# Kernel optimization log

Measured on AMD Instinct MI355X. Metric: run time of the kernel, lower is better.

## Reference

```python
import jax, jax.numpy as jnp
import numpy as np

N, D, N_CLASSES = 8192, 512, 128
POS_MARGIN = 1.0  # default path: sample_method=None, Dynamic_margin=None


def setup_inputs() -> dict:
    key = jax.random.key(0)
    k1, k2 = jax.random.split(key)
    x = jax.random.normal(k1, (N, D), dtype=jnp.float32)
    # metric-learning embeddings are L2-normalized so sim in [-1, 1]
    x = x / jnp.linalg.norm(x, axis=1, keepdims=True)
    targets = jax.random.randint(k2, (N,), 0, N_CLASSES, dtype=jnp.int64)
    return {"inputs": x, "targets": targets, "nonorm": 0}


def reference(inputs, targets, nonorm):
    n = inputs.shape[0]
    sim = jnp.matmul(inputs, inputs.T)                      # [n, n]
    same = targets[:, None] == targets[None, :]             # [n, n]
    pos_mask = same & (sim < POS_MARGIN)                    # drops self-sim == 1
    neg_mask = ~same

    # per-row masked log-sum-exp (sort in original is irrelevant to the sums)
    pos_sum = jnp.sum(jnp.where(pos_mask, jnp.exp(1.0 - sim), 0.0), axis=1)
    neg_sum = jnp.sum(jnp.where(neg_mask, jnp.exp(sim), 0.0), axis=1)
    pos_loss = jnp.log(pos_sum)
    neg_loss = jnp.log(neg_sum)

    has_neg = jnp.any(neg_mask, axis=1)                     # rows w/o negs are skipped
    loss = jnp.sum(jnp.where(has_neg, pos_loss + neg_loss, 0.0)) / n
    prec = jnp.mean(1.0 - has_neg.astype(jnp.float32))      # fraction of skipped rows

    # torch code reports means of the LAST row's pos/neg pairs
    last_pos = pos_mask[-1]
    last_neg = neg_mask[-1]
    mean_pos_sim = jnp.sum(jnp.where(last_pos, sim[-1], 0.0)) / jnp.sum(last_pos)
    mean_neg_sim = jnp.sum(jnp.where(last_neg, sim[-1], 0.0)) / jnp.sum(last_neg)
    return loss, prec, mean_pos_sim, mean_neg_sim
```

## Files before the change

kernel.cpp:

```cpp
#include <hip/hip_runtime.h>
#include <math.h>

#define N_ 8192
#define D_ 512
#define NC_ 128
#define T32 32
#define BK_ 64
#define KSTEPS 8

typedef __attribute__((ext_vector_type(8))) short bf16x8;
typedef __attribute__((ext_vector_type(4))) float f32x4;
typedef __attribute__((ext_vector_type(4))) unsigned short us4;

static __device__ __forceinline__ unsigned short f2bf(float f) {
    union { float f; unsigned u; } c; c.f = f;
    unsigned u = c.u;
    u += 0x7fffu + ((u >> 16) & 1u);
    return (unsigned short)(u >> 16);
}

__global__ __launch_bounds__(256) void k_pre(const float* __restrict__ x,
                                             unsigned short* __restrict__ xb,
                                             const int* __restrict__ tg,
                                             double* __restrict__ sim_last,
                                             int* __restrict__ hist32) {
    const int bid = blockIdx.x;
    const int tid = threadIdx.x;
    if (bid < 4096) {
        int i = bid * 256 + tid;
        float4 v = reinterpret_cast<const float4*>(x)[i];
        us4 o = { f2bf(v.x), f2bf(v.y), f2bf(v.z), f2bf(v.w) };
        reinterpret_cast<us4*>(xb)[i] = o;
    } else if (bid < 6144) {
        int j    = (bid - 4096) * 4 + (tid >> 6);
        int lane = tid & 63;
        const float* xl = x + (size_t)(N_ - 1) * D_;
        const float* xj = x + (size_t)j * D_;
        double acc = 0.0;
#pragma unroll
        for (int it = 0; it < 8; ++it) {
            int k = it * 64 + lane;
            acc += (double)xl[k] * (double)xj[k];
        }
#pragma unroll
        for (int m = 32; m >= 1; m >>= 1) acc += __shfl_xor(acc, m, 64);
        if (lane == 0) sim_last[j] = acc;
    } else {
        __shared__ int lh[NC_];
        int b = bid - 6144;
        if (tid < NC_) lh[tid] = 0;
        __syncthreads();
        atomicAdd(&lh[tg[b * 256 + tid]], 1);
        __syncthreads();
        if (tid < NC_) hist32[b * NC_ + tid] = lh[tid];
    }
}

__global__ __launch_bounds__(512, 2) void k_main(const unsigned short* __restrict__ xb,
                                                 const int* __restrict__ tg,
                                                 float* __restrict__ bufP,
                                                 float* __restrict__ bufN) {
    __shared__ alignas(16) unsigned short As0_[2 * 256 * 64];
    __shared__ alignas(16) unsigned short Bs0_[2 * 256 * 64];

    const int tid  = threadIdx.x;
    const int w    = tid >> 6;
    const int lane = tid & 63;
    const int q    = lane >> 4;
    const int l15  = lane & 15;
    const int wrow = w >> 2;
    const int wcol = w & 3;

    const int bswz = (blockIdx.x & 7) * 66 + (blockIdx.x >> 3);

    int rem = bswz;
    int it = 0;
    while (rem >= (T32 - it)) { rem -= (T32 - it); it++; }
    const int jt = it + rem;
    const int row0 = it * 256;
    const int col0 = jt * 256;

    auto stage_tile = [&](int p, int kt) {
        const int k0 = kt * BK_;
#pragma unroll
        for (int set = 0; set < 4; ++set) {
            int ls = set * 4096 + tid * 8;
            int r  = ls >> 6;
            int sl = (ls >> 3) & 7;
            int g  = sl ^ (r & 7);
            const unsigned short* ga = xb + (size_t)(row0 + r) * D_ + k0 + g * 8;
            const unsigned short* gb = xb + (size_t)(col0 + r) * D_ + k0 + g * 8;
            __builtin_amdgcn_global_load_lds(
                (const __attribute__((address_space(1))) void*)ga,
                (__attribute__((address_space(3))) void*)(As0_ + p * 16384 + set * 4096 + w * 512),
                16, 0, 0);
            __builtin_amdgcn_global_load_lds(
                (const __attribute__((address_space(1))) void*)gb,
                (__attribute__((address_space(3))) void*)(Bs0_ + p * 16384 + set * 4096 + w * 512),
                16, 0, 0);
        }
    };

    f32x4 acc[8][4];
#pragma unroll
    for (int mi = 0; mi < 8; ++mi)
#pragma unroll
        for (int ni = 0; ni < 4; ++ni)
            acc[mi][ni] = (f32x4){0.f, 0.f, 0.f, 0.f};

    auto compute_kc = [&](int p, int kc) {
        bf16x8 aF[8], bF[4];
#pragma unroll
        for (int mi = 0; mi < 8; ++mi) {
            int rA = wrow * 128 + mi * 16 + l15;
            int sl = (kc * 4 + q) ^ (rA & 7);
            aF[mi] = *reinterpret_cast<const bf16x8*>(As0_ + p * 16384 + rA * 64 + sl * 8);
        }
#pragma unroll
        for (int ni = 0; ni < 4; ++ni) {
            int rB = wcol * 64 + ni * 16 + l15;
            int sl = (kc * 4 + q) ^ (rB & 7);
            bF[ni] = *reinterpret_cast<const bf16x8*>(Bs0_ + p * 16384 + rB * 64 + sl * 8);
        }
        asm volatile("s_waitcnt lgkmcnt(0)" ::: "memory");
        __builtin_amdgcn_sched_barrier(0);
        __builtin_amdgcn_s_setprio(1);
#pragma unroll
        for (int mi = 0; mi < 8; ++mi)
#pragma unroll
            for (int ni = 0; ni < 4; ++ni)
                acc[mi][ni] = __builtin_amdgcn_mfma_f32_16x16x32_bf16(
                    aF[mi], bF[ni], acc[mi][ni], 0, 0, 0);
        __builtin_amdgcn_s_setprio(0);
    };

#define TILE(P, KS, DOSTAGE, VMN)                                         \
    do {                                                                  \
        asm volatile("s_waitcnt vmcnt(" #VMN ")" ::: "memory");           \
        __builtin_amdgcn_s_barrier();                                     \
        __builtin_amdgcn_sched_barrier(0);                                \
        compute_kc(P, 0);                                                 \
        compute_kc(P, 1);                                                 \
        __builtin_amdgcn_s_barrier();                                     \
        if (DOSTAGE) stage_tile(P, (KS) + 2);                             \
    } while (0)

    stage_tile(0, 0);
    stage_tile(1, 1);

    TILE(0, 0, 1, 8);
    TILE(1, 1, 1, 8);
    TILE(0, 2, 1, 8);
    TILE(1, 3, 1, 8);
    TILE(0, 4, 1, 8);
    TILE(1, 5, 1, 8);
    TILE(0, 6, 0, 8);
    TILE(1, 7, 0, 0);
#undef TILE

    int tC[4];
#pragma unroll
    for (int ni = 0; ni < 4; ++ni)
        tC[ni] = tg[col0 + wcol * 64 + ni * 16 + l15];

    float cps[4], cns[4];
#pragma unroll
    for (int ni = 0; ni < 4; ++ni) { cps[ni] = 0.f; cns[ni] = 0.f; }

    float* scr = (float*)As0_;

#pragma unroll
    for (int mi = 0; mi < 8; ++mi) {
        int tRv[4];
#pragma unroll
        for (int r = 0; r < 4; ++r)
            tRv[r] = tg[row0 + wrow * 128 + mi * 16 + q * 4 + r];
        float ps_[4] = {0.f, 0.f, 0.f, 0.f};
        float ns_[4] = {0.f, 0.f, 0.f, 0.f};
#pragma unroll
        for (int ni = 0; ni < 4; ++ni)
#pragma unroll
            for (int r = 0; r < 4; ++r) {
                float s = acc[mi][ni][r];
                bool same = (tRv[r] == tC[ni]);
                float e = __expf(same ? 1.0f - s : s);
                float pe = (same && (s < 1.0f)) ? e : 0.0f;
                float ne = same ? 0.0f : e;
                ps_[r] += pe; ns_[r] += ne;
                cps[ni] += pe; cns[ni] += ne;
            }
#pragma unroll
        for (int r = 0; r < 4; ++r) {
            float p = ps_[r];
            float n = ns_[r];
#pragma unroll
            for (int m = 1; m < 16; m <<= 1) {
                p += __shfl_xor(p, m, 64);
                n += __shfl_xor(n, m, 64);
            }
            if (l15 == 0) {
                int rloc = wrow * 128 + mi * 16 + q * 4 + r;
                scr[wcol * 256 + rloc]        = p;
                scr[1024 + wcol * 256 + rloc] = n;
            }
        }
    }

#pragma unroll
    for (int ni = 0; ni < 4; ++ni) {
        float p = cps[ni];
        float n = cns[ni];
        p += __shfl_xor(p, 16, 64); p += __shfl_xor(p, 32, 64);
        n += __shfl_xor(n, 16, 64); n += __shfl_xor(n, 32, 64);
        if (q == 0) {
            int cloc = wcol * 64 + ni * 16 + l15;
            scr[2048 + wrow * 256 + cloc] = p;
            scr[2560 + wrow * 256 + cloc] = n;
        }
    }
    __syncthreads();

    if (tid < 256) {
        int r = tid;
        size_t off = ((size_t)it * T32 + jt) * 256 + r;
        bufP[off] = scr[r] + scr[256 + r] + scr[512 + r] + scr[768 + r];
        bufN[off] = scr[1024 + r] + scr[1280 + r] + scr[1536 + r] + scr[1792 + r];
    } else if (jt != it) {
        int c = tid - 256;
        size_t off = ((size_t)jt * T32 + it) * 256 + c;
        bufP[off] = scr[2048 + c] + scr[2304 + c];
        bufN[off] = scr[2560 + c] + scr[2816 + c];
    }
}

__global__ __launch_bounds__(512) void k_post(const float* __restrict__ bufP,
                                              const float* __restrict__ bufN,
                                              const int* __restrict__ tg,
                                              const int* __restrict__ hist32,
                                              const double* __restrict__ sim_last,
                                              double* __restrict__ dpart,
                                              int* __restrict__ ipart) {
    __shared__ float sv[512];
    __shared__ int lh[NC_];
    __shared__ double Rd[512], Pd[512], Nd[512];
    __shared__ int Ri[512], Pc[512], Nc[512];
    const int rt  = blockIdx.x;
    const int tid = threadIdx.x;
    const int half = tid >> 8;
    const int r    = tid & 255;
    const float* buf  = half ? bufN : bufP;
    const float* base = buf + (size_t)rt * T32 * 256 + r;
    float s = 0.f;
#pragma unroll
    for (int o = 0; o < T32; ++o) s += base[o * 256];
    sv[tid] = s;
    if (tid < NC_) {
        int a = 0;
#pragma unroll
        for (int b = 0; b < 32; ++b) a += hist32[b * NC_ + tid];
        lh[tid] = a;
    }
    __syncthreads();
    double rd = 0.0, pd = 0.0, nd = 0.0;
    int ri = 0, pc = 0, nc = 0;
    if (tid < 256) {
        int row = rt * 256 + tid;
        bool ok = lh[tg[row]] < N_;
        rd = ok ? (double)(logf(sv[tid]) + logf(sv[256 + tid])) : 0.0;
        ri = ok ? 0 : 1;
        double sl = sim_last[row];
        int tlast = tg[N_ - 1];
        if (tg[row] == tlast) { if (sl < 1.0) { pd = sl; pc = 1; } }
        else                  { nd = sl; nc = 1; }
    }
    Rd[tid] = rd; Pd[tid] = pd; Nd[tid] = nd;
    Ri[tid] = ri; Pc[tid] = pc; Nc[tid] = nc;
    __syncthreads();
    for (int st = 256; st >= 1; st >>= 1) {
        if (tid < st) {
            Rd[tid] += Rd[tid + st]; Pd[tid] += Pd[tid + st]; Nd[tid] += Nd[tid + st];
            Ri[tid] += Ri[tid + st]; Pc[tid] += Pc[tid + st]; Nc[tid] += Nc[tid + st];
        }
        __syncthreads();
    }
    if (tid == 0) {
        dpart[rt] = Rd[0]; dpart[32 + rt] = Pd[0]; dpart[64 + rt] = Nd[0];
        ipart[rt] = Ri[0]; ipart[32 + rt] = Pc[0]; ipart[64 + rt] = Nc[0];
    }
}

__global__ __launch_bounds__(64) void k_fin(const double* __restrict__ dpart,
                                            const int* __restrict__ ipart,
                                            float* __restrict__ out) {
    int tid = threadIdx.x;
    double rd = tid < 32 ? dpart[tid]      : 0.0;
    double pd = tid < 32 ? dpart[32 + tid] : 0.0;
    double nd = tid < 32 ? dpart[64 + tid] : 0.0;
    int    ri = tid < 32 ? ipart[tid]      : 0;
    int    pc = tid < 32 ? ipart[32 + tid] : 0;
    int    nc = tid < 32 ? ipart[64 + tid] : 0;
#pragma unroll
    for (int m = 32; m >= 1; m >>= 1) {
        rd += __shfl_xor(rd, m, 64); pd += __shfl_xor(pd, m, 64);
        nd += __shfl_xor(nd, m, 64);
        ri += __shfl_xor(ri, m, 64); pc += __shfl_xor(pc, m, 64);
        nc += __shfl_xor(nc, m, 64);
    }
    if (tid == 0) {
        out[0] = (float)(rd / (double)N_);
        out[1] = (float)ri / (float)N_;
        out[2] = (float)(pd / (double)pc);
        out[3] = (float)(nd / (double)nc);
    }
}

extern "C" void kernel_launch(void* const* d_in, const int* in_sizes, int n_in,
                              void* d_out, int out_size, void* d_ws, size_t ws_size,
                              hipStream_t stream) {
    const float* x  = (const float*)d_in[0];
    const int*   tg = (const int*)d_in[1];
    char* ws = (char*)d_ws;

    unsigned short* xb = (unsigned short*)ws;
    const size_t XB = (size_t)N_ * D_ * 2;
    float*  bufP     = (float*)(ws + XB);
    float*  bufN     = (float*)(ws + XB + (1u << 20));
    double* sim_last = (double*)(ws + XB + (2u << 20));
    int*    hist32   = (int*)(ws + XB + (2u << 20) + 65536);
    double* dpart    = (double*)(ws + XB + (2u << 20) + 65536 + 16384);
    int*    ipart    = (int*)(ws + XB + (2u << 20) + 65536 + 16384 + 1024);

    const int nblk_tri = T32 * (T32 + 1) / 2;

    hipLaunchKernelGGL(k_pre, dim3(4096 + 2048 + 32), dim3(256), 0, stream,
                       x, xb, tg, sim_last, hist32);
    hipLaunchKernelGGL(k_main, dim3(nblk_tri), dim3(512), 0, stream, xb, tg, bufP, bufN);
    hipLaunchKernelGGL(k_post, dim3(T32), dim3(512), 0, stream,
                       bufP, bufN, tg, hist32, sim_last, dpart, ipart);
    hipLaunchKernelGGL(k_fin, dim3(1), dim3(64), 0, stream, dpart, ipart, (float*)d_out);
}
```

Before: 157.4 us.

## Fuse final reduction into k_post via atomics and relax k_main launch bounds

```diff
diff --git a/kernel.cpp b/kernel.cpp
--- a/kernel.cpp
+++ b/kernel.cpp
@@ -23,9 +23,18 @@
                                              unsigned short* __restrict__ xb,
                                              const int* __restrict__ tg,
                                              double* __restrict__ sim_last,
-                                             int* __restrict__ hist32) {
+                                             int* __restrict__ hist32,
+                                             double* __restrict__ gd,
+                                             int* __restrict__ gi) {
     const int bid = blockIdx.x;
     const int tid = threadIdx.x;
+    if (bid == 0 && tid == 0) {
+        atomicExch((unsigned long long*)&gd[0], 0ull);
+        atomicExch((unsigned long long*)&gd[1], 0ull);
+        atomicExch((unsigned long long*)&gd[2], 0ull);
+        atomicExch(&gi[0], 0); atomicExch(&gi[1], 0);
+        atomicExch(&gi[2], 0); atomicExch(&gi[3], 0);
+    }
     if (bid < 4096) {
         int i = bid * 256 + tid;
         float4 v = reinterpret_cast<const float4*>(x)[i];
@@ -56,7 +65,7 @@
     }
 }
 
-__global__ __launch_bounds__(512, 2) void k_main(const unsigned short* __restrict__ xb,
+__global__ __launch_bounds__(512, 1) void k_main(const unsigned short* __restrict__ xb,
                                                  const int* __restrict__ tg,
                                                  float* __restrict__ bufP,
                                                  float* __restrict__ bufN) {
@@ -142,6 +151,7 @@
         compute_kc(P, 0);                                                 \
         compute_kc(P, 1);                                                 \
         __builtin_amdgcn_s_barrier();                                     \
+        __builtin_amdgcn_sched_barrier(0);                                \
         if (DOSTAGE) stage_tile(P, (KS) + 2);                             \
     } while (0)
 
@@ -233,84 +243,86 @@
     }
 }
 
-__global__ __launch_bounds__(512) void k_post(const float* __restrict__ bufP,
+__global__ __launch_bounds__(256) void k_post(const float* __restrict__ bufP,
                                               const float* __restrict__ bufN,
                                               const int* __restrict__ tg,
                                               const int* __restrict__ hist32,
                                               const double* __restrict__ sim_last,
-                                              double* __restrict__ dpart,
-                                              int* __restrict__ ipart) {
-    __shared__ float sv[512];
+                                              double* __restrict__ gd,
+                                              int* __restrict__ gi,
+                                              float* __restrict__ out) {
     __shared__ int lh[NC_];
-    __shared__ double Rd[512], Pd[512], Nd[512];
-    __shared__ int Ri[512], Pc[512], Nc[512];
-    const int rt  = blockIdx.x;
+    __shared__ float sv[256];
+    __shared__ double Rd[256], Pd[256], Nd[256];
+    __shared__ int Ri[256], Pc[256], Nc[256];
+    const int t   = blockIdx.x;
     const int tid = threadIdx.x;
-    const int half = tid >> 8;
-    const int r    = tid & 255;
+
+    if (tid < NC_) {
+        int a = 0;
+#pragma unroll
+        for (int b = 0; b < 32; ++b) a += hist32[b * NC_ + tid];
+        lh[tid] = a;
+    }
+
+    const int half = tid >> 7;
+    const int r    = tid & 127;
+    const int rt   = t >> 1;
+    const int r256 = (t & 1) * 128 + r;
     const float* buf  = half ? bufN : bufP;
-    const float* base = buf + (size_t)rt * T32 * 256 + r;
+    const float* base = buf + (size_t)rt * T32 * 256 + r256;
     float s = 0.f;
 #pragma unroll
     for (int o = 0; o < T32; ++o) s += base[o * 256];
     sv[tid] = s;
-    if (tid < NC_) {
-        int a = 0;
-#pragma unroll
-        for (int b = 0; b < 32; ++b) a += hist32[b * NC_ + tid];
-        lh[tid] = a;
-    }
     __syncthreads();
+
     double rd = 0.0, pd = 0.0, nd = 0.0;
     int ri = 0, pc = 0, nc = 0;
-    if (tid < 256) {
-        int row = rt * 256 + tid;
+    if (tid < 128) {
+        int row = t * 128 + tid;
         bool ok = lh[tg[row]] < N_;
-        rd = ok ? (double)(logf(sv[tid]) + logf(sv[256 + tid])) : 0.0;
+        rd = ok ? (double)(logf(sv[tid]) + logf(sv[128 + tid])) : 0.0;
         ri = ok ? 0 : 1;
         double sl = sim_last[row];
         int tlast = tg[N_ - 1];
         if (tg[row] == tlast) { if (sl < 1.0) { pd = sl; pc = 1; } }
         else                  { nd = sl; nc = 1; }
     }
-    Rd[tid] = rd; Pd[tid] = pd; Nd[tid] = nd;
-    Ri[tid] = ri; Pc[tid] = pc; Nc[tid] = nc;
+
+    Rd[tid] = rd; Ri[tid] = ri;
+    Pd[tid] = pd; Pc[tid] = pc;
+    Nd[tid] = nd; Nc[tid] = nc;
     __syncthreads();
-    for (int st = 256; st >= 1; st >>= 1) {
+    for (int st = 128; st >= 1; st >>= 1) {
         if (tid < st) {
             Rd[tid] += Rd[tid + st]; Pd[tid] += Pd[tid + st]; Nd[tid] += Nd[tid + st];
             Ri[tid] += Ri[tid + st]; Pc[tid] += Pc[tid + st]; Nc[tid] += Nc[tid + st];
         }
         __syncthreads();
     }
+
     if (tid == 0) {
-        dpart[rt] = Rd[0]; dpart[32 + rt] = Pd[0]; dpart[64 + rt] = Nd[0];
-        ipart[rt] = Ri[0]; ipart[32 + rt] = Pc[0]; ipart[64 + rt] = Nc[0];
-    }
-}
-
-__global__ __launch_bounds__(64) void k_fin(const double* __restrict__ dpart,
-                                            const int* __restrict__ ipart,
-                                            float* __restrict__ out) {
-    int tid = threadIdx.x;
-    double rd = tid < 32 ? dpart[tid]      : 0.0;
-    double pd = tid < 32 ? dpart[32 + tid] : 0.0;
-    double nd = tid < 32 ? dpart[64 + tid] : 0.0;
-    int    ri = tid < 32 ? ipart[tid]      : 0;
-    int    pc = tid < 32 ? ipart[32 + tid] : 0;
-    int    nc = tid < 32 ? ipart[64 + tid] : 0;
-#pragma unroll
-    for (int m = 32; m >= 1; m >>= 1) {
-        rd += __shfl_xor(rd, m, 64); pd += __shfl_xor(pd, m, 64);
-        nd += __shfl_xor(nd, m, 64);
-        ri += __shfl_xor(ri, m, 64); pc += __shfl_xor(pc, m, 64);
-        nc += __shfl_xor(nc, m, 64);
-    }
-    if (tid == 0) {
-        out[0] = (float)(rd / (double)N_);
-        out[1] = (float)ri / (float)N_;
-        out[2] = (float)(pd / (double)pc);
-        out[3] = (float)(nd / (double)nc);
+        atomicAdd(&gd[0], Rd[0]);
+        atomicAdd(&gd[1], Pd[0]);
+        atomicAdd(&gd[2], Nd[0]);
+        atomicAdd(&gi[0], Ri[0]);
+        atomicAdd(&gi[1], Pc[0]);
+        atomicAdd(&gi[2], Nc[0]);
+        __threadfence();
+        int old = atomicAdd(&gi[3], 1);
+        if (old == 63) {
+            double A = atomicAdd(&gd[0], 0.0);
+            double B = atomicAdd(&gd[1], 0.0);
+            double C = atomicAdd(&gd[2], 0.0);
+            int U = atomicAdd(&gi[0], 0);
+            int V = atomicAdd(&gi[1], 0);
+            int Y = atomicAdd(&gi[2], 0);
+            out[0] = (float)(A / (double)N_);
+            out[1] = (float)U / (float)N_;
+            out[2] = (float)(B / (double)V);
+            out[3] = (float)(C / (double)Y);
+        }
     }
 }
 
@@ -323,19 +335,18 @@
 
     unsigned short* xb = (unsigned short*)ws;
     const size_t XB = (size_t)N_ * D_ * 2;
-    float*  bufP     = (float*)(ws + XB);
-    float*  bufN     = (float*)(ws + XB + (1u << 20));
+    float*  bufP = (float*)(ws + XB);
+    float*  bufN = (float*)(ws + XB + (1u << 20));
     double* sim_last = (double*)(ws + XB + (2u << 20));
     int*    hist32   = (int*)(ws + XB + (2u << 20) + 65536);
-    double* dpart    = (double*)(ws + XB + (2u << 20) + 65536 + 16384);
-    int*    ipart    = (int*)(ws + XB + (2u << 20) + 65536 + 16384 + 1024);
+    double* gd   = (double*)(ws + XB + (2u << 20) + 65536 + 16384);
+    int*    gi   = (int*)(ws + XB + (2u << 20) + 65536 + 16384 + 64);
 
     const int nblk_tri = T32 * (T32 + 1) / 2;
 
     hipLaunchKernelGGL(k_pre, dim3(4096 + 2048 + 32), dim3(256), 0, stream,
-                       x, xb, tg, sim_last, hist32);
+                       x, xb, tg, sim_last, hist32, gd, gi);
     hipLaunchKernelGGL(k_main, dim3(nblk_tri), dim3(512), 0, stream, xb, tg, bufP, bufN);
-    hipLaunchKernelGGL(k_post, dim3(T32), dim3(512), 0, stream,
-                       bufP, bufN, tg, hist32, sim_last, dpart, ipart);
-    hipLaunchKernelGGL(k_fin, dim3(1), dim3(64), 0, stream, dpart, ipart, (float*)d_out);
-}
+    hipLaunchKernelGGL(k_post, dim3(64), dim3(256), 0, stream,
+                       bufP, bufN, tg, hist32, sim_last, gd, gi, (float*)d_out);
+}
```

Result: slower. 162.0 us (+3.0%).
